# Kernel tuning notes

Measured on AMD Instinct MI355X. Metric: run time of the kernel, lower is better.

Reference implementation:

```python
import jax, jax.numpy as jnp
import numpy as np

BATCH, SEQ, D_IN, UNITS = 32, 2048, 256, 256


def setup_inputs() -> dict:
    key = jax.random.key(0)
    k1, k2, k3 = jax.random.split(key, 3)
    x = jax.random.normal(k1, (BATCH, SEQ, D_IN), dtype=jnp.float32)
    # packed gate weights in order [i, f, g, o]
    W = jax.random.normal(k2, (D_IN, 4 * UNITS), dtype=jnp.float32) * (1.0 / np.sqrt(D_IN))
    U = jax.random.normal(k3, (UNITS, 4 * UNITS), dtype=jnp.float32) * (1.0 / np.sqrt(UNITS))
    b = jnp.zeros((4 * UNITS,), dtype=jnp.float32)
    return {"x": x, "W": W, "U": U, "b": b}


def reference(x, W, U, b):
    """LSTM layer: zero init states, loop over time, return all hidden states.
    x: [B, T, D]; W: [D, 4H]; U: [H, 4H]; b: [4H] -> out: [B, T, H]."""
    B = x.shape[0]
    H = U.shape[0]
    # Precompute the input contribution for all timesteps in one big GEMM.
    xW = jnp.einsum('btd,dg->btg', x, W) + b  # [B, T, 4H]

    def step(carry, xw_t):
        h, c = carry
        gates = xw_t + h @ U  # [B, 4H]
        i, f, g, o = jnp.split(gates, 4, axis=-1)
        i = jax.nn.sigmoid(i)
        f = jax.nn.sigmoid(f)
        g = jnp.tanh(g)
        o = jax.nn.sigmoid(o)
        c = f * c + i * g
        h = o * jnp.tanh(c)
        return (h, c), h

    h0 = jnp.zeros((B, H), dtype=x.dtype)
    c0 = jnp.zeros((B, H), dtype=x.dtype)
    # scan over time: xW transposed to [T, B, 4H]
    _, hs = jax.lax.scan(step, (h0, c0), jnp.swapaxes(xW, 0, 1))
    return jnp.swapaxes(hs, 0, 1)  # [B, T, H]
```

## Files before the change

kernel.cpp:

```cpp
#include <hip/hip_runtime.h>
#include <hip/hip_fp16.h>

typedef _Float16 f16;
typedef _Float16 f16x2 __attribute__((ext_vector_type(2)));
typedef _Float16 f16x8 __attribute__((ext_vector_type(8)));
typedef float f32x4 __attribute__((ext_vector_type(4)));
typedef unsigned int u32;

#define BATCH 32
#define SEQT  2048
#define DIN   256
#define HU    256
#define G4    1024
#define MROWS (BATCH*SEQT)

#define WS_XW 0
#define WS_XH 134217728UL
#define WS_WT 167772160UL
#define WS_UP 168296448UL
#define WS_NEED 168820736UL

__global__ void pack_u(const float* __restrict__ U, u32* __restrict__ upk4) {
    int idx = blockIdx.x * 256 + threadIdx.x;
    int p = idx >> 10, j = idx & 1023;
    f16x2 h;
    h.x = (f16)U[(2 * p) * G4 + j];
    h.y = (f16)U[(2 * p + 1) * G4 + j];
    upk4[(((p >> 2) * 1024 + j) << 2) + (p & 3)] = __builtin_bit_cast(u32, h);
}

__global__ void conv_x(const float* __restrict__ x, f16* __restrict__ xh) {
    int idx = blockIdx.x * 256 + threadIdx.x;
    int row = idx >> 5, c = idx & 31;
    const float4* src = (const float4*)(x + row * 256 + c * 8);
    float4 v0 = src[0], v1 = src[1];
    f16x8 o;
    o[0] = (f16)v0.x; o[1] = (f16)v0.y; o[2] = (f16)v0.z; o[3] = (f16)v0.w;
    o[4] = (f16)v1.x; o[5] = (f16)v1.y; o[6] = (f16)v1.z; o[7] = (f16)v1.w;
    *(f16x8*)(xh + row * 256 + c * 8) = o;
}

__global__ void conv_w(const float* __restrict__ W, f16* __restrict__ wt) {
    int idx = blockIdx.x * 256 + threadIdx.x;
    int j = idx >> 5, c = idx & 31;
    f16x8 o;
#pragma unroll
    for (int i = 0; i < 8; ++i) o[i] = (f16)W[(c * 8 + i) * G4 + j];
    *(f16x8*)(wt + j * 256 + c * 8) = o;
}

__launch_bounds__(256)
__global__ void gemm_xw(const f16* __restrict__ xh, const f16* __restrict__ wt,
                        const float* __restrict__ bias, f16* __restrict__ xw) {
    __shared__ __align__(16) f16 As[128 * 256];
    __shared__ __align__(16) f16 Bs[128 * 256];
    int mt = blockIdx.x, nt = blockIdx.y;
    int t = threadIdx.x, lane = t & 63, w = t >> 6;

    const uint4* Ag = (const uint4*)(xh + (size_t)mt * 128 * 256);
    const uint4* Bg = (const uint4*)(wt + (size_t)nt * 128 * 256);
#pragma unroll
    for (int i = 0; i < 16; ++i) {
        int o16 = t + i * 256;
        int row = o16 >> 5, c = o16 & 31;
        uint4 va = Ag[o16];
        uint4 vb = Bg[o16];
        int sw = c ^ (row & 7);
        *(uint4*)((char*)As + row * 512 + sw * 16) = va;
        *(uint4*)((char*)Bs + row * 512 + sw * 16) = vb;
    }
    __syncthreads();

    int wr = w >> 1, wc = w & 1;
    f32x4 acc[4][4];
#pragma unroll
    for (int mi = 0; mi < 4; ++mi)
#pragma unroll
        for (int ni = 0; ni < 4; ++ni) acc[mi][ni] = (f32x4){0.f, 0.f, 0.f, 0.f};

    int rA = lane & 15;
    int kg = lane >> 4;
#pragma unroll
    for (int ks = 0; ks < 8; ++ks) {
        f16x8 af[4], bf[4];
#pragma unroll
        for (int mi = 0; mi < 4; ++mi) {
            int row = wr * 64 + mi * 16 + rA;
            int c = ks * 4 + kg;
            af[mi] = *(const f16x8*)((const char*)As + row * 512 + ((c ^ (row & 7)) * 16));
        }
#pragma unroll
        for (int ni = 0; ni < 4; ++ni) {
            int row = wc * 64 + ni * 16 + rA;
            int c = ks * 4 + kg;
            bf[ni] = *(const f16x8*)((const char*)Bs + row * 512 + ((c ^ (row & 7)) * 16));
        }
#pragma unroll
        for (int mi = 0; mi < 4; ++mi)
#pragma unroll
            for (int ni = 0; ni < 4; ++ni)
                acc[mi][ni] = __builtin_amdgcn_mfma_f32_16x16x32_f16(af[mi], bf[ni], acc[mi][ni], 0, 0, 0);
    }

    int r4 = (lane >> 4) * 4, cc = lane & 15;
    float bv[4];
#pragma unroll
    for (int ni = 0; ni < 4; ++ni) bv[ni] = bias[nt * 128 + wc * 64 + ni * 16 + cc];
#pragma unroll
    for (int mi = 0; mi < 4; ++mi)
#pragma unroll
        for (int ni = 0; ni < 4; ++ni)
#pragma unroll
            for (int q = 0; q < 4; ++q) {
                int grow = mt * 128 + wr * 64 + mi * 16 + r4 + q;
                int gcol = nt * 128 + wc * 64 + ni * 16 + cc;
                xw[(size_t)grow * 1024 + gcol] = (f16)(acc[mi][ni][q] + bv[ni]);
            }
}

__device__ __forceinline__ float fdot2u(u32 u, u32 h, float acc) {
    return __builtin_amdgcn_fdot2(__builtin_bit_cast(f16x2, u),
                                  __builtin_bit_cast(f16x2, h), acc, false);
}
__device__ __forceinline__ float sigm(float x) {
    return 1.0f / (1.0f + __expf(-x));
}
__device__ __forceinline__ float tanh_f(float x) {
    x = fminf(fmaxf(x, -15.0f), 15.0f);
    float e = __expf(2.0f * x);
    return (e - 1.0f) / (e + 1.0f);
}


#define DECLC(c) uint4 uc_##c;
#define LOADC(c) do { uc_##c = upk4[(c) * 1024 + t]; } while (0)
#define CHR(c) do {                                \
    uint4 hv = *(const uint4*)&hpair[4*(c)];       \
    a0 = fdot2u(uc_##c.x, hv.x, a0);               \
    a1 = fdot2u(uc_##c.y, hv.y, a1);               \
    a2 = fdot2u(uc_##c.z, hv.z, a2);               \
    a3 = fdot2u(uc_##c.w, hv.w, a3);               \
} while (0)

__launch_bounds__(1024)
__global__ void lstm_rec(const uint4* __restrict__ upk4, const f16* __restrict__ xw,
                         float* __restrict__ out) {
    __shared__ __align__(16) u32 ulds[1024 * 36];
    __shared__ __align__(16) u32 hpair[128];
    __shared__ __align__(16) float gbuf[1024];

    int b = blockIdx.x, t = threadIdx.x;

    DECLC(0)  DECLC(1)  DECLC(2)  DECLC(3)  DECLC(4)  DECLC(5)
    DECLC(6)  DECLC(7)  DECLC(8)  DECLC(9)  DECLC(10) DECLC(11)
    DECLC(12) DECLC(13) DECLC(14) DECLC(15) DECLC(16) DECLC(17)
    DECLC(18) DECLC(19) DECLC(20) DECLC(21) DECLC(22)

    LOADC(0);  LOADC(1);  LOADC(2);  LOADC(3);  LOADC(4);  LOADC(5);
    LOADC(6);  LOADC(7);  LOADC(8);  LOADC(9);  LOADC(10); LOADC(11);
    LOADC(12); LOADC(13); LOADC(14); LOADC(15); LOADC(16); LOADC(17);
    LOADC(18); LOADC(19); LOADC(20); LOADC(21); LOADC(22);

#pragma unroll
    for (int ch = 0; ch < 9; ++ch) {
        uint4 v = upk4[(23 + ch) * 1024 + t];
        *(uint4*)&ulds[t * 36 + ch * 4] = v;
    }
    if (t < 128) hpair[t] = 0u;

    float c_state = 0.0f;
    const f16* xp = xw + (size_t)b * SEQT * G4;
    float* op = out + (size_t)b * SEQT * HU;
    f16 xa = xp[t];
    __syncthreads();

    for (int st = 0; st < SEQT; ++st) {
        float a0 = (float)xa, a1 = 0.f, a2 = 0.f, a3 = 0.f;
        if (st < SEQT - 1) xa = xp[G4 + t];
        xp += G4;

        CHR(0);  CHR(1);  CHR(2);  CHR(3);  CHR(4);  CHR(5);
        CHR(6);  CHR(7);  CHR(8);  CHR(9);  CHR(10); CHR(11);
        CHR(12); CHR(13); CHR(14); CHR(15); CHR(16); CHR(17);
        CHR(18); CHR(19); CHR(20); CHR(21); CHR(22);

#pragma unroll
        for (int ch = 0; ch < 9; ++ch) {
            uint4 hv = *(const uint4*)&hpair[92 + ch * 4];
            uint4 u4 = *(const uint4*)&ulds[t * 36 + ch * 4];
            a0 = fdot2u(u4.x, hv.x, a0);
            a1 = fdot2u(u4.y, hv.y, a1);
            a2 = fdot2u(u4.z, hv.z, a2);
            a3 = fdot2u(u4.w, hv.w, a3);
        }
        float a = (a0 + a1) + (a2 + a3);

        float act = ((t >> 8) == 2) ? tanh_f(a) : sigm(a);
        gbuf[t] = act;
        __syncthreads();

        if (t < 256) {
            float gi = gbuf[t];
            float gf = gbuf[256 + t];
            float gg = gbuf[512 + t];
            float go = gbuf[768 + t];
            c_state = gf * c_state + gi * gg;
            float h = go * tanh_f(c_state);
            op[t] = h;
            ((f16*)hpair)[t] = (f16)h;
        }
        op += HU;
        __syncthreads();
    }
}

extern "C" void kernel_launch(void* const* d_in, const int* in_sizes, int n_in,
                              void* d_out, int out_size, void* d_ws, size_t ws_size,
                              hipStream_t stream) {
    const float* x    = (const float*)d_in[0];
    const float* W    = (const float*)d_in[1];
    const float* U    = (const float*)d_in[2];
    const float* bias = (const float*)d_in[3];
    float* out = (float*)d_out;

    if (ws_size < WS_NEED) return;
    char* ws = (char*)d_ws;
    f16* xw    = (f16*)(ws + WS_XW);
    f16* xh    = (f16*)(ws + WS_XH);
    f16* wt    = (f16*)(ws + WS_WT);
    u32* upk4  = (u32*)(ws + WS_UP);

    pack_u<<<512, 256, 0, stream>>>(U, upk4);
    conv_x<<<8192, 256, 0, stream>>>(x, xh);
    conv_w<<<128, 256, 0, stream>>>(W, wt);
    gemm_xw<<<dim3(512, 8), 256, 0, stream>>>(xh, wt, bias, xw);
    lstm_rec<<<32, 1024, 0, stream>>>((const uint4*)upk4, xw, out);
}
```

Measured before the change: 4.156 ms.

## Split each batch's LSTM recurrence across four workgroups with global flag sync

```diff
diff --git a/kernel.cpp b/kernel.cpp
--- a/kernel.cpp
+++ b/kernel.cpp
@@ -18,7 +18,9 @@
 #define WS_XH 134217728UL
 #define WS_WT 167772160UL
 #define WS_UP 168296448UL
-#define WS_NEED 168820736UL
+#define WS_HX 168820736UL
+#define WS_FLG 168853504UL
+#define WS_NEED 168857600UL
 
 __global__ void pack_u(const float* __restrict__ U, u32* __restrict__ upk4) {
     int idx = blockIdx.x * 256 + threadIdx.x;
@@ -132,85 +134,112 @@
 }
 
 
-#define DECLC(c) uint4 uc_##c;
-#define LOADC(c) do { uc_##c = upk4[(c) * 1024 + t]; } while (0)
-#define CHR(c) do {                                \
-    uint4 hv = *(const uint4*)&hpair[4*(c)];       \
-    a0 = fdot2u(uc_##c.x, hv.x, a0);               \
-    a1 = fdot2u(uc_##c.y, hv.y, a1);               \
-    a2 = fdot2u(uc_##c.z, hv.z, a2);               \
-    a3 = fdot2u(uc_##c.w, hv.w, a3);               \
-} while (0)
-
-__launch_bounds__(1024)
+__launch_bounds__(256)
 __global__ void lstm_rec(const uint4* __restrict__ upk4, const f16* __restrict__ xw,
-                         float* __restrict__ out) {
-    __shared__ __align__(16) u32 ulds[1024 * 36];
+                         float* __restrict__ out, u32* hx, int* flg) {
+    __shared__ __align__(16) u32 ulds[256 * 128];
     __shared__ __align__(16) u32 hpair[128];
-    __shared__ __align__(16) float gbuf[1024];
-
-    int b = blockIdx.x, t = threadIdx.x;
-
-    DECLC(0)  DECLC(1)  DECLC(2)  DECLC(3)  DECLC(4)  DECLC(5)
-    DECLC(6)  DECLC(7)  DECLC(8)  DECLC(9)  DECLC(10) DECLC(11)
-    DECLC(12) DECLC(13) DECLC(14) DECLC(15) DECLC(16) DECLC(17)
-    DECLC(18) DECLC(19) DECLC(20) DECLC(21) DECLC(22)
-
-    LOADC(0);  LOADC(1);  LOADC(2);  LOADC(3);  LOADC(4);  LOADC(5);
-    LOADC(6);  LOADC(7);  LOADC(8);  LOADC(9);  LOADC(10); LOADC(11);
-    LOADC(12); LOADC(13); LOADC(14); LOADC(15); LOADC(16); LOADC(17);
-    LOADC(18); LOADC(19); LOADC(20); LOADC(21); LOADC(22);
-
-#pragma unroll
-    for (int ch = 0; ch < 9; ++ch) {
-        uint4 v = upk4[(23 + ch) * 1024 + t];
-        *(uint4*)&ulds[t * 36 + ch * 4] = v;
+    __shared__ __align__(16) float gbuf[256];
+
+    int wg = blockIdx.x, b = wg >> 2, q = wg & 3;
+    int t = threadIdx.x;
+    int g = t >> 6, ul = t & 63;
+    int gcol = g * 256 + q * 64 + ul;
+
+    for (int c = 0; c < 32; ++c) {
+        uint4 v = upk4[c * 1024 + gcol];
+        *(uint4*)&ulds[t * 128 + ((c ^ (t & 7)) << 2)] = v;
     }
     if (t < 128) hpair[t] = 0u;
+
+    u32* hx_b  = hx + b * 128;
+    int* flg_b = flg + b * 32;
 
     float c_state = 0.0f;
     const f16* xp = xw + (size_t)b * SEQT * G4;
-    float* op = out + (size_t)b * SEQT * HU;
-    f16 xa = xp[t];
+    float* op = out + (size_t)b * SEQT * HU + q * 64;
+    f16 xa = xp[gcol];
     __syncthreads();
 
     for (int st = 0; st < SEQT; ++st) {
+        u32* hx_rd = hx_b + (((st + 1) & 1) << 12);
+        u32* hx_wr = hx_b + ((st & 1) << 12);
+
         float a0 = (float)xa, a1 = 0.f, a2 = 0.f, a3 = 0.f;
-        if (st < SEQT - 1) xa = xp[G4 + t];
+        if (st < SEQT - 1) xa = xp[G4 + gcol];
         xp += G4;
 
-        CHR(0);  CHR(1);  CHR(2);  CHR(3);  CHR(4);  CHR(5);
-        CHR(6);  CHR(7);  CHR(8);  CHR(9);  CHR(10); CHR(11);
-        CHR(12); CHR(13); CHR(14); CHR(15); CHR(16); CHR(17);
-        CHR(18); CHR(19); CHR(20); CHR(21); CHR(22);
-
-#pragma unroll
-        for (int ch = 0; ch < 9; ++ch) {
-            uint4 hv = *(const uint4*)&hpair[92 + ch * 4];
-            uint4 u4 = *(const uint4*)&ulds[t * 36 + ch * 4];
+#pragma unroll
+        for (int i = 0; i < 8; ++i) {
+            int c = q * 8 + i;
+            uint4 hv = *(const uint4*)&hpair[c << 2];
+            uint4 u4 = *(const uint4*)&ulds[t * 128 + ((c ^ (t & 7)) << 2)];
             a0 = fdot2u(u4.x, hv.x, a0);
             a1 = fdot2u(u4.y, hv.y, a1);
             a2 = fdot2u(u4.z, hv.z, a2);
             a3 = fdot2u(u4.w, hv.w, a3);
         }
+
+        if (t < 3) {
+            int p = t + (t >= q);
+            int spins = 0;
+            while (__hip_atomic_load(&flg_b[p * 8], __ATOMIC_ACQUIRE,
+                                     __HIP_MEMORY_SCOPE_AGENT) < st &&
+                   spins < (1 << 22)) {
+                __builtin_amdgcn_s_sleep(1);
+                ++spins;
+            }
+        }
+        __syncthreads();
+        if (t < 96) {
+            int p = t >> 5, d = t & 31;
+            int pidx = p + (p >= q);
+            hpair[pidx * 32 + d] =
+                __hip_atomic_load(&hx_rd[pidx * 32 + d], __ATOMIC_RELAXED,
+                                  __HIP_MEMORY_SCOPE_AGENT);
+        }
+        __syncthreads();
+
+#pragma unroll
+        for (int j = 0; j < 4; ++j) {
+            if (j == q) continue;
+#pragma unroll
+            for (int i = 0; i < 8; ++i) {
+                int c = j * 8 + i;
+                uint4 hv = *(const uint4*)&hpair[c << 2];
+                uint4 u4 = *(const uint4*)&ulds[t * 128 + ((c ^ (t & 7)) << 2)];
+                a0 = fdot2u(u4.x, hv.x, a0);
+                a1 = fdot2u(u4.y, hv.y, a1);
+                a2 = fdot2u(u4.z, hv.z, a2);
+                a3 = fdot2u(u4.w, hv.w, a3);
+            }
+        }
         float a = (a0 + a1) + (a2 + a3);
 
-        float act = ((t >> 8) == 2) ? tanh_f(a) : sigm(a);
+        float act = (g == 2) ? tanh_f(a) : sigm(a);
         gbuf[t] = act;
         __syncthreads();
 
-        if (t < 256) {
+        if (t < 64) {
             float gi = gbuf[t];
-            float gf = gbuf[256 + t];
-            float gg = gbuf[512 + t];
-            float go = gbuf[768 + t];
+            float gf = gbuf[64 + t];
+            float gg = gbuf[128 + t];
+            float go = gbuf[192 + t];
             c_state = gf * c_state + gi * gg;
             float h = go * tanh_f(c_state);
             op[t] = h;
-            ((f16*)hpair)[t] = (f16)h;
+            ((f16*)hpair)[q * 64 + t] = (f16)h;
         }
         op += HU;
         __syncthreads();
+
+        if (t < 32)
+            __hip_atomic_store(&hx_wr[q * 32 + t], hpair[q * 32 + t],
+                               __ATOMIC_RELAXED, __HIP_MEMORY_SCOPE_AGENT);
+        __syncthreads();
+        if (t == 0)
+            __hip_atomic_store(&flg_b[q * 8], st + 1, __ATOMIC_RELEASE,
+                               __HIP_MEMORY_SCOPE_AGENT);
     }
 }
 
@@ -229,10 +258,14 @@
     f16* xh    = (f16*)(ws + WS_XH);
     f16* wt    = (f16*)(ws + WS_WT);
     u32* upk4  = (u32*)(ws + WS_UP);
+    u32* hx    = (u32*)(ws + WS_HX);
+    int* flg   = (int*)(ws + WS_FLG);
+
+    hipMemsetAsync(ws + WS_HX, 0, WS_NEED - WS_HX, stream);
 
     pack_u<<<512, 256, 0, stream>>>(U, upk4);
     conv_x<<<8192, 256, 0, stream>>>(x, xh);
     conv_w<<<128, 256, 0, stream>>>(W, wt);
     gemm_xw<<<dim3(512, 8), 256, 0, stream>>>(xh, wt, bias, xw);
-    lstm_rec<<<32, 1024, 0, stream>>>((const uint4*)upk4, xw, out);
-}
+    lstm_rec<<<128, 256, 0, stream>>>((const uint4*)upk4, xw, out, hx, flg);
+}
```

New measurement: 6.637 ms. +59.7%, slower.
